# Kernel tuning notes

Hardware: AMD Instinct MI355X
Metric: run time of the kernel (lower is better)

## Reference

```python
import jax, jax.numpy as jnp
from jax import lax
import numpy as np

PARAM_SPECS = [
    ("w1", (16, 15, 5, 5)), ("b1", (16,)),
    ("w2", (32, 16, 3, 3)), ("b2", (32,)),
    ("w3", (32, 32, 3, 3)), ("b3", (32,)),
    ("w4", (32, 32, 3, 3)), ("b4", (32,)),
    ("w5", (64, 32, 3, 3)), ("b5", (64,)),
    ("w6", (32, 96, 3, 3)), ("b6", (32,)),
    ("w7", (32, 64, 3, 3)), ("b7", (32,)),
    ("w8", (32, 64, 3, 3)), ("b8", (32,)),
    ("w9", (64, 48, 3, 3)), ("b9", (64,)),
    ("wi", (16, 15, 3, 3)), ("bi", (16,)),
    ("wo", (3, 16, 3, 3)), ("bo", (3,)),
]


def conv2d(x, w, b, pad):
    y = lax.conv_general_dilated(x, w, (1, 1), [(pad, pad), (pad, pad)],
                                 dimension_numbers=("NCHW", "OIHW", "NCHW"))
    return y + b[None, :, None, None]


def maxpool2(x):
    return lax.reduce_window(x, -jnp.inf, lax.max, (1, 1, 2, 2), (1, 1, 2, 2), "VALID")


def upsample(x, hw):
    # bilinear, half-pixel centers == torch align_corners=False
    B, C = x.shape[:2]
    return jax.image.resize(x, (B, C, hw[0], hw[1]), method="bilinear")


def dcnn(img, p):
    x1 = jax.nn.relu(conv2d(img, p["w1"], p["b1"], 2))
    x2 = jax.nn.relu(conv2d(maxpool2(x1), p["w2"], p["b2"], 1))
    x3 = jax.nn.relu(conv2d(maxpool2(x2), p["w3"], p["b3"], 1))
    x4 = jax.nn.relu(conv2d(maxpool2(x3), p["w4"], p["b4"], 1))
    x5 = jax.nn.relu(conv2d(maxpool2(x4), p["w5"], p["b5"], 1))
    x6 = jax.nn.relu(conv2d(jnp.concatenate([upsample(x5, x4.shape[-2:]), x4], 1), p["w6"], p["b6"], 1))
    x7 = jax.nn.relu(conv2d(jnp.concatenate([upsample(x6, x3.shape[-2:]), x3], 1), p["w7"], p["b7"], 1))
    x8 = jax.nn.relu(conv2d(jnp.concatenate([upsample(x7, x2.shape[-2:]), x2], 1), p["w8"], p["b8"], 1))
    x9 = conv2d(jnp.concatenate([upsample(x8, x1.shape[-2:]), x1], 1), p["w9"], p["b9"], 1)
    return x9


def lrnn_op(X, P, axis, flip):
    # h_k = (1-P_k)*X_k + P_k*h_{k-1}, scanned along `axis`.
    # For reverse directions the torch code stacks hidden states in scan
    # order (spatially flipped) -> flip inputs, scan forward, keep order.
    if flip:
        X = jnp.flip(X, axis)
        P = jnp.flip(P, axis)
    xs = jnp.moveaxis(X, axis, 0)  # [L, B, 16, n]
    ps = jnp.moveaxis(P, axis, 0)

    def step(h, xp):
        x, p = xp
        h = (1.0 - p) * x + p * h
        return h, h

    h0 = jnp.zeros_like(xs[0])
    _, ys = lax.scan(step, h0, (xs, ps))
    return jnp.moveaxis(ys, 0, axis)


def lrnn_layer(x_in, fm):
    dirs = [(0, 3, False), (0, 3, True), (16, 2, False), (16, 2, True),
            (32, 3, False), (32, 3, True), (48, 2, False), (48, 2, True)]
    outs = [lrnn_op(x_in, fm[:, c:c + 16], axis, flip) for (c, axis, flip) in dirs]
    return jnp.max(jnp.stack(outs, axis=1), axis=1)


def setup_inputs() -> dict:
    key = jax.random.key(0)
    ks = jax.random.split(key, len(PARAM_SPECS) + 1)
    inp = {"img": jax.random.normal(ks[0], (8, 15, 256, 256), jnp.float32)}
    for i, (name, shape) in enumerate(PARAM_SPECS):
        inp[name] = jax.random.normal(ks[i + 1], shape, jnp.float32) * 0.05
    return inp


def reference(img, w1, b1, w2, b2, w3, b3, w4, b4, w5, b5, w6, b6, w7, b7,
              w8, b8, w9, b9, wi, bi, wo, bo):
    p = dict(w1=w1, b1=b1, w2=w2, b2=b2, w3=w3, b3=b3, w4=w4, b4=b4, w5=w5,
             b5=b5, w6=w6, b6=b6, w7=w7, b7=b7, w8=w8, b8=b8, w9=w9, b9=b9)
    fm = jnp.tanh(dcnn(img, p))          # [B,64,H,W]
    x_in = conv2d(img, wi, bi, 1)         # [B,16,H,W]
    out = lrnn_layer(x_in, fm)            # [B,16,H,W]
    return jax.nn.sigmoid(conv2d(out, wo, bo, 1))  # [B,3,H,W]
```

## Files before the change

kernel.cpp:

```cpp
#include <hip/hip_runtime.h>
#include <math.h>

typedef __attribute__((ext_vector_type(8)))  short bf16x8;
typedef __attribute__((ext_vector_type(8)))  unsigned short u16x8;
typedef __attribute__((ext_vector_type(16))) float f32x16;

__device__ __forceinline__ unsigned short f2bf(float f) {
    unsigned u = __float_as_uint(f);
    unsigned r = (u + 0x7FFFu + ((u >> 16) & 1u)) >> 16;
    return (unsigned short)r;
}
__device__ __forceinline__ float bf2f(unsigned short h) {
    return __uint_as_float(((unsigned)h) << 16);
}
__device__ __forceinline__ unsigned pack2(unsigned short a, unsigned short b) {
    return (unsigned)a | ((unsigned)b << 16);
}
__device__ __forceinline__ float fast_tanh(float x) {
    float e = __expf(2.f * x);
    return 1.f - 2.f / (e + 1.f);
}

__device__ __forceinline__ void bilin_setup(int y, int x, int Hi, int Wi,
                                            int& i00, int& i01, int& i10, int& i11,
                                            float& wy, float& wx)
{
    float fy = 0.5f * y - 0.25f;
    float fx = 0.5f * x - 0.25f;
    float y0f = floorf(fy), x0f = floorf(fx);
    wy = fy - y0f; wx = fx - x0f;
    int yA = (int)y0f, xA = (int)x0f;
    int yB = yA + 1, xB = xA + 1;
    yA = yA < 0 ? 0 : (yA > Hi - 1 ? Hi - 1 : yA);
    yB = yB < 0 ? 0 : (yB > Hi - 1 ? Hi - 1 : yB);
    xA = xA < 0 ? 0 : (xA > Wi - 1 ? Wi - 1 : xA);
    xB = xB < 0 ? 0 : (xB > Wi - 1 ? Wi - 1 : xB);
    i00 = yA * Wi + xA; i01 = yA * Wi + xB;
    i10 = yB * Wi + xA; i11 = yB * Wi + xB;
}

__device__ __forceinline__ void up2_setup(int v, int Hi, int& i0, int& i1, float& w)
{
    int a = (v - 1) >> 1;
    i0 = a < 0 ? 0 : a;
    int b = a + 1;
    i1 = b > Hi - 1 ? Hi - 1 : b;
    w = (v & 1) ? 0.25f : 0.75f;
}

__device__ __forceinline__ u16x8 bilin8(const unsigned short* __restrict__ sb,
                                        int i00, int i01, int i10, int i11,
                                        float wy, float wx, int stride)
{
    u16x8 v00 = *(const u16x8*)(sb + (size_t)i00 * stride);
    u16x8 v01 = *(const u16x8*)(sb + (size_t)i01 * stride);
    u16x8 v10 = *(const u16x8*)(sb + (size_t)i10 * stride);
    u16x8 v11 = *(const u16x8*)(sb + (size_t)i11 * stride);
    float w00 = (1.f - wy) * (1.f - wx), w01 = (1.f - wy) * wx;
    float w10 = wy * (1.f - wx),         w11 = wy * wx;
    u16x8 r;
#pragma unroll
    for (int j = 0; j < 8; ++j)
        r[j] = f2bf(w00 * bf2f(v00[j]) + w01 * bf2f(v01[j]) +
                    w10 * bf2f(v10[j]) + w11 * bf2f(v11[j]));
    return r;
}

__device__ const float ALPH[3][2][3][3] = {
    { { {0.f,0.f,0.f},      {0.f,1.f,0.f},       {0.f,0.75f,0.25f} },
      { {0.f,1.f,0.f},      {0.f,0.75f,0.25f},   {0.f,0.25f,0.75f} } },
    { { {0.75f,0.25f,0.f},  {0.25f,0.75f,0.f},   {0.f,0.75f,0.25f} },
      { {0.25f,0.75f,0.f},  {0.f,0.75f,0.25f},   {0.f,0.25f,0.75f} } },
    { { {0.75f,0.25f,0.f},  {0.25f,0.75f,0.f},   {0.f,1.f,0.f} },
      { {0.25f,0.75f,0.f},  {0.f,1.f,0.f},       {0.f,0.f,0.f} } }
};

__global__ void imgT_bf16(const float* __restrict__ img, unsigned short* __restrict__ dst)
{
    int idx = blockIdx.x * 256 + threadIdx.x;
    if (idx >= 8 * 256 * 256) return;
    int x = idx & 255, y = (idx >> 8) & 255, b = idx >> 16;
    unsigned short v[16];
#pragma unroll
    for (int c = 0; c < 15; ++c)
        v[c] = f2bf(img[(size_t)(b * 15 + c) * 65536 + y * 256 + x]);
    v[15] = 0;
    uint4 lo = make_uint4(pack2(v[0], v[1]), pack2(v[2], v[3]), pack2(v[4], v[5]), pack2(v[6], v[7]));
    uint4 hi = make_uint4(pack2(v[8], v[9]), pack2(v[10], v[11]), pack2(v[12], v[13]), pack2(v[14], v[15]));
    *(uint4*)(dst + (size_t)idx * 16)     = lo;
    *(uint4*)(dst + (size_t)idx * 16 + 8) = hi;
}

__device__ __forceinline__ void pack33(const float* __restrict__ w,
                                       unsigned short* __restrict__ dst,
                                       int i, int Cin, int Cout)
{
    int KST = Cin >> 4, MT = Cout >> 5;
    int j = i & 7;
    int lane = (i >> 3) & 63;
    int t = i >> 9;
    int mt = t % MT; t /= MT;
    int kst = t % KST;
    int s = t / KST;
    int oc = mt * 32 + (lane & 31);
    int ci = kst * 16 + (lane >> 5) * 8 + j;
    dst[i] = f2bf(w[(oc * Cin + ci) * 9 + s]);
}

__global__ void wprep_mega(const float* __restrict__ w9, const float* __restrict__ w8,
                           const float* __restrict__ w1, const float* __restrict__ wi,
                           const float* __restrict__ wo, const float* __restrict__ w2,
                           const float* __restrict__ w3, const float* __restrict__ w4,
                           const float* __restrict__ w5, const float* __restrict__ w6,
                           const float* __restrict__ w7,
                           unsigned short* __restrict__ wpk9, unsigned short* __restrict__ wpk8,
                           unsigned short* __restrict__ wpk1, unsigned short* __restrict__ wpki,
                           unsigned short* __restrict__ wpko, unsigned short* __restrict__ wpk2,
                           unsigned short* __restrict__ wpk3, unsigned short* __restrict__ wpk4,
                           unsigned short* __restrict__ wpk5, unsigned short* __restrict__ wpk6,
                           unsigned short* __restrict__ wpk7, unsigned short* __restrict__ wpk9e,
                           unsigned short* __restrict__ wpk8e)
{
    int idx = blockIdx.x * 256 + threadIdx.x;
    if (idx < 27648)       pack33(w9, wpk9, idx, 48, 64);
    else if (idx < 46080)  pack33(w8, wpk8, idx - 27648, 64, 32);
    else if (idx < 58880) {
        int i = idx - 46080;
        int j = i & 7;
        int lane = (i >> 3) & 63;
        int s = i >> 9;
        int oc = lane & 31;
        int ci = (lane >> 5) * 8 + j;
        float v = 0.f;
        if (oc < 16 && ci < 15) v = w1[((oc * 15 + ci) * 5 + s / 5) * 5 + s % 5];
        wpk1[i] = f2bf(v);
    } else if (idx < 63488) {
        int i = idx - 58880;
        int j = i & 7;
        int lane = (i >> 3) & 63;
        int s = i >> 9;
        int oc = lane & 31;
        int ci = (lane >> 5) * 8 + j;
        float v = 0.f;
        if (oc < 16 && ci < 15) v = wi[((oc * 15 + ci) * 3 + s / 3) * 3 + s % 3];
        wpki[i] = f2bf(v);
    } else if (idx < 68096) {
        int i = idx - 63488;
        int j = i & 7;
        int lane = (i >> 3) & 63;
        int s = i >> 9;
        int oc = lane & 31;
        int ci = (lane >> 5) * 8 + j;
        float v = 0.f;
        if (oc < 3) v = wo[((oc * 16 + ci) * 3 + s / 3) * 3 + s % 3];
        wpko[i] = f2bf(v);
    }
    else if (idx < 72704)  pack33(w2, wpk2, idx - 68096, 16, 32);
    else if (idx < 81920)  pack33(w3, wpk3, idx - 72704, 32, 32);
    else if (idx < 91136)  pack33(w4, wpk4, idx - 81920, 32, 32);
    else if (idx < 109568) pack33(w5, wpk5, idx - 91136, 32, 64);
    else if (idx < 137216) pack33(w6, wpk6, idx - 109568, 96, 32);
    else if (idx < 155648) pack33(w7, wpk7, idx - 137216, 64, 32);
    else if (idx < 266240) {
        int i = idx - 155648;
        int j = i & 7;
        int lane = (i >> 3) & 63;
        int t = i >> 9;
        int half = t & 1; t >>= 1;
        int kst  = t & 1; t >>= 1;
        int s    = t % 9; t /= 9;
        int py   = t & 1;
        int cls  = t >> 1;
        int dr = s / 3, dx = s % 3;
        int oc = half * 32 + (lane & 31);
        int ci = kst * 16 + (lane >> 5) * 8 + j;
        float v = 0.f;
#pragma unroll
        for (int dy = 0; dy < 3; ++dy)
            v += ALPH[cls][py][dy][dr] * w9[((oc * 48 + ci) * 3 + dy) * 3 + dx];
        wpk9e[i] = f2bf(v);
    }
    else if (idx < 321536) {
        int i = idx - 266240;
        int j = i & 7;
        int lane = (i >> 3) & 63;
        int t = i >> 9;
        int kst = t & 1; t >>= 1;
        int s   = t % 9; t /= 9;
        int py  = t & 1;
        int cls = t >> 1;
        int dr = s / 3, dx = s % 3;
        int oc = lane & 31;
        int ci = kst * 16 + (lane >> 5) * 8 + j;
        float v = 0.f;
#pragma unroll
        for (int dy = 0; dy < 3; ++dy)
            v += ALPH[cls][py][dy][dr] * w8[((oc * 64 + ci) * 3 + dy) * 3 + dx];
        wpk8e[i] = f2bf(v);
    }
}

template<int CIN, int COUT, int H, int W, int ROWS, int POOL>
__global__ __launch_bounds__(256)
void convN_mfma(const unsigned short* __restrict__ in,
                const unsigned short* __restrict__ wpk,
                const float* __restrict__ bias,
                unsigned short* __restrict__ out)
{
    constexpr int G = CIN / 8;
    constexpr int KST = CIN / 16;
    constexpr int MT = COUT / 32;
    constexpr int TR = ROWS + 2;
    constexpr int TWd = W + 2;
    constexpr int PS = TR * TWd * 8 + 8;
    __shared__ __align__(16) unsigned short smem[G * PS];

    const int tid  = threadIdx.x;
    const int lane = tid & 63;
    const int wv   = tid >> 6;
    const int q    = lane >> 5;
    const int y0   = blockIdx.x * ROWS;
    const int b    = blockIdx.y;

    for (int i = tid; i < G * TR * TWd; i += 256) {
        int g = i % G;
        int u = (i / G) % TWd;
        int t = i / (G * TWd);
        int yg = y0 + t - 1, xg = u - 1;
        u16x8 v = {0, 0, 0, 0, 0, 0, 0, 0};
        if (yg >= 0 && yg < H && xg >= 0 && xg < W) {
            if (POOL) {
                const unsigned short* q0 =
                    in + (((size_t)(b * 2 * H + 2 * yg) * 2 * W + 2 * xg) * CIN + g * 8);
                u16x8 a0 = *(const u16x8*)q0;
                u16x8 a1 = *(const u16x8*)(q0 + CIN);
                u16x8 a2 = *(const u16x8*)(q0 + (size_t)2 * W * CIN);
                u16x8 a3 = *(const u16x8*)(q0 + (size_t)2 * W * CIN + CIN);
#pragma unroll
                for (int j = 0; j < 8; ++j)
                    v[j] = f2bf(fmaxf(fmaxf(bf2f(a0[j]), bf2f(a1[j])),
                                      fmaxf(bf2f(a2[j]), bf2f(a3[j]))));
            } else {
                v = *(const u16x8*)(in + (((size_t)(b * H + yg) * W + xg) * CIN + g * 8));
            }
        }
        *(u16x8*)(&smem[g * PS + (t * TWd + u) * 8]) = v;
    }
    __syncthreads();

    const int p = wv * 32 + (lane & 31);
    const int r = p / W;
    const int x = p % W;

    f32x16 acc[MT];
#pragma unroll
    for (int mt = 0; mt < MT; ++mt)
#pragma unroll
        for (int i = 0; i < 16; ++i) acc[mt][i] = 0.f;

    const unsigned short* wbase = wpk + lane * 8;

#pragma unroll
    for (int s = 0; s < 9; ++s) {
        const int dy = s / 3, dx = s % 3;
#pragma unroll
        for (int kst = 0; kst < KST; ++kst) {
            const int g = kst * 2 + q;
            bf16x8 bfrag = *(const bf16x8*)(&smem[g * PS + ((r + dy) * TWd + (x + dx)) * 8]);
#pragma unroll
            for (int mt = 0; mt < MT; ++mt) {
                bf16x8 a = *(const bf16x8*)(wbase + ((s * KST + kst) * MT + mt) * 512);
                acc[mt] = __builtin_amdgcn_mfma_f32_32x32x16_bf16(a, bfrag, acc[mt], 0, 0, 0);
            }
        }
    }

    size_t base = ((size_t)(b * H + y0 + r) * W + x) * COUT;
#pragma unroll
    for (int mt = 0; mt < MT; ++mt)
#pragma unroll
        for (int rg = 0; rg < 4; ++rg) {
            int oc = mt * 32 + 8 * rg + 4 * q;
            unsigned short s0 = f2bf(fmaxf(acc[mt][rg * 4 + 0] + bias[oc + 0], 0.f));
            unsigned short s1 = f2bf(fmaxf(acc[mt][rg * 4 + 1] + bias[oc + 1], 0.f));
            unsigned short s2 = f2bf(fmaxf(acc[mt][rg * 4 + 2] + bias[oc + 2], 0.f));
            unsigned short s3 = f2bf(fmaxf(acc[mt][rg * 4 + 3] + bias[oc + 3], 0.f));
            *(uint2*)(out + base + oc) = make_uint2(pack2(s0, s1), pack2(s2, s3));
        }
}

template<int UPC, int CSKIP, int COUT, int H, int W, int ROWS>
__global__ __launch_bounds__(256)
void convU_mfma(const unsigned short* __restrict__ up,
                const unsigned short* __restrict__ skip,
                const unsigned short* __restrict__ wpk,
                const float* __restrict__ bias,
                unsigned short* __restrict__ out)
{
    constexpr int CIN = UPC + CSKIP;
    constexpr int G = CIN / 8;
    constexpr int GU = UPC / 8;
    constexpr int KST = CIN / 16;
    constexpr int MT = COUT / 32;
    constexpr int TR = ROWS + 2;
    constexpr int TWd = W + 2;
    constexpr int PS = TR * TWd * 8 + 8;
    __shared__ __align__(16) unsigned short smem[G * PS];

    const int tid  = threadIdx.x;
    const int lane = tid & 63;
    const int wv   = tid >> 6;
    const int q    = lane >> 5;
    const int y0   = blockIdx.x * ROWS;
    const int b    = blockIdx.y;

    for (int i = tid; i < G * TR * TWd; i += 256) {
        int g = i % G;
        int u = (i / G) % TWd;
        int t = i / (G * TWd);
        int yg = y0 + t - 1, xg = u - 1;
        u16x8 v = {0, 0, 0, 0, 0, 0, 0, 0};
        if (yg >= 0 && yg < H && xg >= 0 && xg < W) {
            if (g < GU) {
                int i00, i01, i10, i11; float wy, wx;
                bilin_setup(yg, xg, H / 2, W / 2, i00, i01, i10, i11, wy, wx);
                v = bilin8(up + (size_t)b * (H / 2) * (W / 2) * UPC + g * 8,
                           i00, i01, i10, i11, wy, wx, UPC);
            } else {
                v = *(const u16x8*)(skip + (((size_t)(b * H + yg) * W + xg) * CSKIP
                                            + (g - GU) * 8));
            }
        }
        *(u16x8*)(&smem[g * PS + (t * TWd + u) * 8]) = v;
    }
    __syncthreads();

    const int p = wv * 32 + (lane & 31);
    const int r = p / W;
    const int x = p % W;

    f32x16 acc[MT];
#pragma unroll
    for (int mt = 0; mt < MT; ++mt)
#pragma unroll
        for (int i = 0; i < 16; ++i) acc[mt][i] = 0.f;

    const unsigned short* wbase = wpk + lane * 8;

#pragma unroll
    for (int s = 0; s < 9; ++s) {
        const int dy = s / 3, dx = s % 3;
#pragma unroll
        for (int kst = 0; kst < KST; ++kst) {
            const int g = kst * 2 + q;
            bf16x8 bfrag = *(const bf16x8*)(&smem[g * PS + ((r + dy) * TWd + (x + dx)) * 8]);
#pragma unroll
            for (int mt = 0; mt < MT; ++mt) {
                bf16x8 a = *(const bf16x8*)(wbase + ((s * KST + kst) * MT + mt) * 512);
                acc[mt] = __builtin_amdgcn_mfma_f32_32x32x16_bf16(a, bfrag, acc[mt], 0, 0, 0);
            }
        }
    }

    size_t base = ((size_t)(b * H + y0 + r) * W + x) * COUT;
#pragma unroll
    for (int mt = 0; mt < MT; ++mt)
#pragma unroll
        for (int rg = 0; rg < 4; ++rg) {
            int oc = mt * 32 + 8 * rg + 4 * q;
            unsigned short s0 = f2bf(fmaxf(acc[mt][rg * 4 + 0] + bias[oc + 0], 0.f));
            unsigned short s1 = f2bf(fmaxf(acc[mt][rg * 4 + 1] + bias[oc + 1], 0.f));
            unsigned short s2 = f2bf(fmaxf(acc[mt][rg * 4 + 2] + bias[oc + 2], 0.f));
            unsigned short s3 = f2bf(fmaxf(acc[mt][rg * 4 + 3] + bias[oc + 3], 0.f));
            *(uint2*)(out + base + oc) = make_uint2(pack2(s0, s1), pack2(s2, s3));
        }
}

__global__ __launch_bounds__(256)
void conv1i_mfma(const unsigned short* __restrict__ imgT,
                 const unsigned short* __restrict__ wpk1,
                 const unsigned short* __restrict__ wpki,
                 const float* __restrict__ b1, const float* __restrict__ bi,
                 unsigned short* __restrict__ x1t, unsigned short* __restrict__ xin)
{
    __shared__ __align__(16) unsigned short smem[2 * 5 * 132 * 8];

    const int tid  = threadIdx.x;
    const int lane = tid & 63;
    const int wv   = tid >> 6;
    const int n    = lane & 31;
    const int q    = lane >> 5;
    const int y    = blockIdx.x >> 1;
    const int x0   = (blockIdx.x & 1) * 128;
    const int b    = blockIdx.y;

    for (int i = tid; i < 5 * 132 * 2; i += 256) {
        int r   = i / 264;
        int rem = i - r * 264;
        int xi  = rem >> 1;
        int g   = rem & 1;
        int yg = y + r - 2;
        int xg = x0 - 2 + xi;
        uint4 v = make_uint4(0, 0, 0, 0);
        if (yg >= 0 && yg < 256 && xg >= 0 && xg < 256)
            v = *(const uint4*)(imgT + (((size_t)(b * 256 + yg) * 256 + xg) * 16 + g * 8));
        *(uint4*)(&smem[((g * 5 + r) * 132 + xi) * 8]) = v;
    }
    __syncthreads();

    f32x16 acc1, acci;
#pragma unroll
    for (int i = 0; i < 16; ++i) { acc1[i] = 0.f; acci[i] = 0.f; }

    const int pxl = wv * 32 + n;
    const unsigned short* wb1 = wpk1 + lane * 8;
    const unsigned short* wbi = wpki + lane * 8;

#pragma unroll
    for (int s = 0; s < 25; ++s) {
        const int dy = s / 5, dx = s % 5;
        bf16x8 bfrag = *(const bf16x8*)(&smem[((q * 5 + dy) * 132 + pxl + dx) * 8]);
        bf16x8 a = *(const bf16x8*)(wb1 + s * 512);
        acc1 = __builtin_amdgcn_mfma_f32_32x32x16_bf16(a, bfrag, acc1, 0, 0, 0);
    }
#pragma unroll
    for (int s = 0; s < 9; ++s) {
        const int dy = s / 3, dx = s % 3;
        bf16x8 bfrag = *(const bf16x8*)(&smem[((q * 5 + dy + 1) * 132 + pxl + dx + 1) * 8]);
        bf16x8 a = *(const bf16x8*)(wbi + s * 512);
        acci = __builtin_amdgcn_mfma_f32_32x32x16_bf16(a, bfrag, acci, 0, 0, 0);
    }

    const int px = x0 + pxl;
    size_t base1 = ((size_t)(b * 256 + y) * 256 + px) * 16;
#pragma unroll
    for (int rg = 0; rg < 2; ++rg) {
        int oc = 8 * rg + 4 * q;
        unsigned short s0 = f2bf(fmaxf(acc1[rg * 4 + 0] + b1[oc + 0], 0.f));
        unsigned short s1 = f2bf(fmaxf(acc1[rg * 4 + 1] + b1[oc + 1], 0.f));
        unsigned short s2 = f2bf(fmaxf(acc1[rg * 4 + 2] + b1[oc + 2], 0.f));
        unsigned short s3 = f2bf(fmaxf(acc1[rg * 4 + 3] + b1[oc + 3], 0.f));
        *(uint2*)(x1t + base1 + oc) = make_uint2(pack2(s0, s1), pack2(s2, s3));
    }
#pragma unroll
    for (int reg = 0; reg < 8; ++reg) {
        int row = (reg & 3) + 8 * (reg >> 2) + 4 * q;
        xin[((size_t)(b * 16 + row) * 256 + y) * 256 + px] = f2bf(acci[reg] + bi[row]);
    }
}

__global__ __launch_bounds__(256)
void conv8_mfma(const unsigned short* __restrict__ x7t,
                const unsigned short* __restrict__ x2t,
                const unsigned short* __restrict__ wpk8,
                const unsigned short* __restrict__ wpk8e,
                const float* __restrict__ bias,
                unsigned short* __restrict__ x8t)
{
    constexpr int PSU = 3 * 66 * 8 + 8;
    constexpr int PSS = 4 * 66 * 8 + 8;
    constexpr int SOFF = 4 * PSU;
    __shared__ __align__(16) unsigned short smem[4 * PSU + 4 * PSS];

    const int tid  = threadIdx.x;
    const int lane = tid & 63;
    const int wv   = tid >> 6;
    const int n    = lane & 31;
    const int q    = lane >> 5;
    const int x0   = (blockIdx.x & 1) * 64;
    const int yp   = blockIdx.x >> 1;
    const int b    = blockIdx.y;

    for (int i = tid; i < 792 + 1056; i += 256) {
        if (i < 792) {
            int g   = i & 3;
            int rem = i >> 2;
            int xi  = rem % 66;
            int t8  = rem / 66;
            int r   = yp - 1 + t8;
            int xg  = x0 - 1 + xi;
            u16x8 v = {0, 0, 0, 0, 0, 0, 0, 0};
            if (r >= 0 && r < 64 && xg >= 0 && xg < 128) {
                int ix0, ix1; float wx;
                up2_setup(xg, 64, ix0, ix1, wx);
                const unsigned short* S = x7t + ((size_t)(b * 64 + r) * 64) * 32 + g * 8;
                u16x8 a0 = *(const u16x8*)(S + ix0 * 32);
                u16x8 a1 = *(const u16x8*)(S + ix1 * 32);
                float w1x = 1.f - wx;
#pragma unroll
                for (int j = 0; j < 8; ++j)
                    v[j] = f2bf(w1x * bf2f(a0[j]) + wx * bf2f(a1[j]));
            }
            *(u16x8*)(&smem[g * PSU + (t8 * 66 + xi) * 8]) = v;
        } else {
            int jI  = i - 792;
            int g   = jI & 3;
            int rem = jI >> 2;
            int xi  = rem % 66;
            int t   = rem / 66;
            int yg  = 2 * yp + t - 1;
            int xg  = x0 - 1 + xi;
            uint4 v = make_uint4(0, 0, 0, 0);
            if (yg >= 0 && yg < 128 && xg >= 0 && xg < 128)
                v = *(const uint4*)(x2t + (((size_t)(b * 128 + yg) * 128 + xg) * 32 + g * 8));
            *(uint4*)(&smem[SOFF + g * PSS + (t * 66 + xi) * 8]) = v;
        }
    }
    __syncthreads();

    const int rr  = wv >> 1;
    const int pxl = (wv & 1) * 32 + n;

    f32x16 acc;
#pragma unroll
    for (int i = 0; i < 16; ++i) acc[i] = 0.f;

    const int cls = (yp == 0) ? 0 : ((yp == 63) ? 2 : 1);
    const unsigned short* wE = wpk8e + (size_t)(cls * 2 + rr) * 9216 + lane * 8;
    const unsigned short* wS = wpk8 + lane * 8;

#pragma unroll
    for (int s = 0; s < 9; ++s) {
        const int dr = s / 3, dxx = s % 3;
#pragma unroll
        for (int kst = 0; kst < 2; ++kst) {
            const int g = kst * 2 + q;
            bf16x8 bfrag = *(const bf16x8*)(&smem[g * PSU + (dr * 66 + pxl + dxx) * 8]);
            bf16x8 a = *(const bf16x8*)(wE + (s * 2 + kst) * 512);
            acc = __builtin_amdgcn_mfma_f32_32x32x16_bf16(a, bfrag, acc, 0, 0, 0);
        }
#pragma unroll
        for (int kst = 0; kst < 2; ++kst) {
            const int g = kst * 2 + q;
            bf16x8 bfrag = *(const bf16x8*)(&smem[SOFF + g * PSS + ((rr + dr) * 66 + pxl + dxx) * 8]);
            bf16x8 a = *(const bf16x8*)(wS + (s * 4 + kst + 2) * 512);
            acc = __builtin_amdgcn_mfma_f32_32x32x16_bf16(a, bfrag, acc, 0, 0, 0);
        }
    }

    size_t base = ((size_t)(b * 128 + 2 * yp + rr) * 128 + x0 + pxl) * 32;
#pragma unroll
    for (int rg = 0; rg < 4; ++rg) {
        int oc0 = 8 * rg + 4 * q;
        unsigned short s0 = f2bf(fmaxf(acc[rg * 4 + 0] + bias[oc0 + 0], 0.f));
        unsigned short s1 = f2bf(fmaxf(acc[rg * 4 + 1] + bias[oc0 + 1], 0.f));
        unsigned short s2 = f2bf(fmaxf(acc[rg * 4 + 2] + bias[oc0 + 2], 0.f));
        unsigned short s3 = f2bf(fmaxf(acc[rg * 4 + 3] + bias[oc0 + 3], 0.f));
        *(uint2*)(x8t + base + oc0) = make_uint2(pack2(s0, s1), pack2(s2, s3));
    }
}

__global__ __launch_bounds__(256)
void conv9f_mfma(const unsigned short* __restrict__ x8t,
                 const unsigned short* __restrict__ x1t,
                 const unsigned short* __restrict__ wpk,
                 const unsigned short* __restrict__ wpk9e,
                 const float* __restrict__ bias,
                 unsigned short* __restrict__ fm)
{
    constexpr int PS8X = 3 * 66 * 8 + 8;
    constexpr int PS1  = 4 * 66 * 8 + 8;
    constexpr int X1OFF = 4 * PS8X;
    __shared__ __align__(16) unsigned short smem[4 * PS8X + 2 * PS1];

    const int tid  = threadIdx.x;
    const int lane = tid & 63;
    const int wv   = tid >> 6;
    const int n    = lane & 31;
    const int q    = lane >> 5;
    const int x0   = (blockIdx.x & 3) * 64;
    const int yp   = blockIdx.x >> 2;
    const int b    = blockIdx.y;

    for (int i = tid; i < 792 + 528; i += 256) {
        if (i < 792) {
            int g   = i & 3;
            int rem = i >> 2;
            int xi  = rem % 66;
            int t8  = rem / 66;
            int r   = yp - 1 + t8;
            int xg  = x0 - 1 + xi;
            u16x8 v = {0, 0, 0, 0, 0, 0, 0, 0};
            if (r >= 0 && r < 128 && xg >= 0 && xg < 256) {
                int ix0, ix1; float wx;
                up2_setup(xg, 128, ix0, ix1, wx);
                const unsigned short* S = x8t + ((size_t)(b * 128 + r) * 128) * 32 + g * 8;
                u16x8 a0 = *(const u16x8*)(S + ix0 * 32);
                u16x8 a1 = *(const u16x8*)(S + ix1 * 32);
                float w1x = 1.f - wx;
#pragma unroll
                for (int j = 0; j < 8; ++j)
                    v[j] = f2bf(w1x * bf2f(a0[j]) + wx * bf2f(a1[j]));
            }
            *(u16x8*)(&smem[g * PS8X + (t8 * 66 + xi) * 8]) = v;
        } else {
            int jI  = i - 792;
            int g   = jI & 1;
            int rem = jI >> 1;
            int xi  = rem % 66;
            int t   = rem / 66;
            int yg  = 2 * yp + t - 1;
            int xg  = x0 - 1 + xi;
            uint4 v = make_uint4(0, 0, 0, 0);
            if (yg >= 0 && yg < 256 && xg >= 0 && xg < 256)
                v = *(const uint4*)(x1t + (((size_t)(b * 256 + yg) * 256 + xg) * 16 + g * 8));
            *(uint4*)(&smem[X1OFF + g * PS1 + (t * 66 + xi) * 8]) = v;
        }
    }
    __syncthreads();

    const int rr  = wv >> 1;
    const int pxl = (wv & 1) * 32 + n;

    f32x16 acc0, acc1;
#pragma unroll
    for (int i = 0; i < 16; ++i) { acc0[i] = 0.f; acc1[i] = 0.f; }

    const int cls = (yp == 0) ? 0 : ((yp == 127) ? 2 : 1);
    const unsigned short* wE  = wpk9e + (size_t)(cls * 2 + rr) * 18432 + lane * 8;
    const unsigned short* w2b = wpk + lane * 8;

#pragma unroll
    for (int s = 0; s < 9; ++s) {
        const int dr = s / 3, dxx = s % 3;
#pragma unroll
        for (int kst = 0; kst < 2; ++kst) {
            const int g = kst * 2 + q;
            bf16x8 bfrag = *(const bf16x8*)(&smem[g * PS8X + (dr * 66 + pxl + dxx) * 8]);
            bf16x8 a0 = *(const bf16x8*)(wE + ((s * 2 + kst) * 2 + 0) * 512);
            bf16x8 a1 = *(const bf16x8*)(wE + ((s * 2 + kst) * 2 + 1) * 512);
            acc0 = __builtin_amdgcn_mfma_f32_32x32x16_bf16(a0, bfrag, acc0, 0, 0, 0);
            acc1 = __builtin_amdgcn_mfma_f32_32x32x16_bf16(a1, bfrag, acc1, 0, 0, 0);
        }
        {
            bf16x8 bfrag = *(const bf16x8*)(&smem[X1OFF + q * PS1 + ((rr + dr) * 66 + pxl + dxx) * 8]);
            bf16x8 a0 = *(const bf16x8*)(w2b + ((s * 3 + 2) * 2 + 0) * 512);
            bf16x8 a1 = *(const bf16x8*)(w2b + ((s * 3 + 2) * 2 + 1) * 512);
            acc0 = __builtin_amdgcn_mfma_f32_32x32x16_bf16(a0, bfrag, acc0, 0, 0, 0);
            acc1 = __builtin_amdgcn_mfma_f32_32x32x16_bf16(a1, bfrag, acc1, 0, 0, 0);
        }
    }

    __syncthreads();
    unsigned short* lout = smem;
    const int pb = rr * 64 + pxl + q * 512;
#pragma unroll
    for (int reg = 0; reg < 16; ++reg) {
        const int rbase = (reg & 3) + 8 * (reg >> 2);
        lout[rbase * 128 + pb]        = f2bf(fast_tanh(acc0[reg] + bias[rbase + 4 * q]));
        lout[(rbase + 32) * 128 + pb] = f2bf(fast_tanh(acc1[reg] + bias[rbase + 4 * q + 32]));
    }
    __syncthreads();

    const size_t fmb = (size_t)b * 64 * 65536 + (size_t)(2 * yp) * 256 + x0;
    for (int i = tid; i < 1024; i += 256) {
        int oc  = i >> 4;
        int p0  = (i & 15) * 8;
        int rr2 = p0 >> 6;
        int pl  = p0 & 63;
        uint4 v = *(const uint4*)(lout + oc * 128 + p0);
        *(uint4*)(fm + fmb + (size_t)oc * 65536 + rr2 * 256 + pl) = v;
    }
}

__device__ __forceinline__ int X2C(int x) { return x + (x >> 5); }

__global__ __launch_bounds__(256)
void lrnn_w_seg(const unsigned short* __restrict__ X, const unsigned short* __restrict__ FM,
                unsigned short* __restrict__ rnnW)
{
    __shared__ float tx[3][16][264];
    __shared__ unsigned short outm[2][16][256];
    __shared__ float segres[2][16][8][4];
    __shared__ float hin[2][16][8][2];

    const int tid = threadIdx.x;
    const int bid = blockIdx.x;
    const int yt = bid & 15;
    const int c  = (bid >> 4) & 15;
    const int b  = bid >> 8;
    const int y0 = yt * 16;

    const size_t xb  = ((size_t)(b * 16 + c) * 256 + y0) * 256;
    const size_t p1b = ((size_t)(b * 64 + c) * 256 + y0) * 256;
    const size_t p2b = ((size_t)(b * 64 + 32 + c) * 256 + y0) * 256;

    for (int i = tid; i < 1536; i += 256) {
        int s = i >> 9;
        int r = i & 511;
        int y = r >> 5;
        int g = r & 31;
        const unsigned short* sp = (s == 0) ? (X + xb) : (s == 1 ? FM + p1b : FM + p2b);
        u16x8 v = *(const u16x8*)(sp + (size_t)y * 256 + g * 8);
        int c0 = X2C(g * 8);
#pragma unroll
        for (int j = 0; j < 8; ++j) tx[s][y][c0 + j] = bf2f(v[j]);
    }
    __syncthreads();

    const int y  = tid & 15;
    const int sg = (tid >> 4) & 7;
    const int d  = tid >> 7;

    {
        float h1 = 0.f, h2 = 0.f, A1 = 1.f, A2 = 1.f;
        if (d == 0) {
            int cs = X2C(sg * 32);
#pragma unroll
            for (int i = 0; i < 32; ++i) {
                float xv = tx[0][y][cs + i], p1 = tx[1][y][cs + i], p2 = tx[2][y][cs + i];
                h1 = fmaf(p1, h1 - xv, xv); A1 *= p1;
                h2 = fmaf(p2, h2 - xv, xv); A2 *= p2;
            }
        } else {
            int cs = X2C(255 - sg * 32);
#pragma unroll
            for (int i = 0; i < 32; ++i) {
                float xv = tx[0][y][cs - i], p1 = tx[1][y][cs - i], p2 = tx[2][y][cs - i];
                h1 = fmaf(p1, h1 - xv, xv); A1 *= p1;
                h2 = fmaf(p2, h2 - xv, xv); A2 *= p2;
            }
        }
        segres[d][y][sg][0] = h1; segres[d][y][sg][1] = A1;
        segres[d][y][sg][2] = h2; segres[d][y][sg][3] = A2;
    }
    __syncthreads();

    if (tid < 32) {
        int yy = tid & 15, dd = tid >> 4;
        float c1 = 0.f, c2 = 0.f;
        for (int s = 0; s < 8; ++s) {
            hin[dd][yy][s][0] = c1;
            hin[dd][yy][s][1] = c2;
            c1 = segres[dd][yy][s][0] + segres[dd][yy][s][1] * c1;
            c2 = segres[dd][yy][s][2] + segres[dd][yy][s][3] * c2;
        }
    }
    __syncthreads();

    {
        float h1 = hin[d][y][sg][0], h2 = hin[d][y][sg][1];
        if (d == 0) {
            int cs = X2C(sg * 32);
            int xs = sg * 32;
#pragma unroll
            for (int i = 0; i < 32; ++i) {
                float xv = tx[0][y][cs + i], p1 = tx[1][y][cs + i], p2 = tx[2][y][cs + i];
                h1 = fmaf(p1, h1 - xv, xv);
                h2 = fmaf(p2, h2 - xv, xv);
                outm[0][y][xs + i] = f2bf(fmaxf(h1, h2));
            }
        } else {
            int cs = X2C(255 - sg * 32);
#pragma unroll
            for (int i = 0; i < 32; ++i) {
                int t = sg * 32 + i;
                float xv = tx[0][y][cs - i], p1 = tx[1][y][cs - i], p2 = tx[2][y][cs - i];
                h1 = fmaf(p1, h1 - xv, xv);
                h2 = fmaf(p2, h2 - xv, xv);
                outm[1][y][t] = f2bf(fmaxf(h1, h2));
            }
        }
    }
    __syncthreads();

    for (int i = tid; i < 4096; i += 256) {
        int x = i & 255, yy = i >> 8;
        float m = fmaxf(bf2f(outm[0][yy][x]), bf2f(outm[1][yy][x]));
        rnnW[xb + (size_t)yy * 256 + x] = f2bf(m);
    }
}

__global__ __launch_bounds__(256)
void lrnn_h_seg(const unsigned short* __restrict__ X, const unsigned short* __restrict__ FM,
                unsigned short* __restrict__ rnnH)
{
    __shared__ float tx[3][264][17];
    __shared__ unsigned short outm[2][256][16];
    __shared__ float segres[2][16][8][4];
    __shared__ float hin[2][16][8][2];

    const int tid = threadIdx.x;
    const int bid = blockIdx.x;
    const int xt = bid & 15;
    const int c  = (bid >> 4) & 15;
    const int b  = bid >> 8;
    const int x0 = xt * 16;

    const size_t xb  = (size_t)(b * 16 + c) * 65536 + x0;
    const size_t p1b = (size_t)(b * 64 + 16 + c) * 65536 + x0;
    const size_t p2b = (size_t)(b * 64 + 48 + c) * 65536 + x0;

    for (int i = tid; i < 1536; i += 256) {
        int s = i >> 9;
        int r = i & 511;
        int y = r >> 1;
        int g = r & 1;
        const unsigned short* sp = (s == 0) ? (X + xb) : (s == 1 ? FM + p1b : FM + p2b);
        u16x8 v = *(const u16x8*)(sp + (size_t)y * 256 + g * 8);
        int pr = y + (y >> 5);
#pragma unroll
        for (int j = 0; j < 8; ++j) tx[s][pr][g * 8 + j] = bf2f(v[j]);
    }
    __syncthreads();

    const int x  = tid & 15;
    const int sg = (tid >> 4) & 7;
    const int d  = tid >> 7;

    {
        float h1 = 0.f, h2 = 0.f, A1 = 1.f, A2 = 1.f;
        if (d == 0) {
            int rs = X2C(sg * 32);
#pragma unroll
            for (int i = 0; i < 32; ++i) {
                float xv = tx[0][rs + i][x], p1 = tx[1][rs + i][x], p2 = tx[2][rs + i][x];
                h1 = fmaf(p1, h1 - xv, xv); A1 *= p1;
                h2 = fmaf(p2, h2 - xv, xv); A2 *= p2;
            }
        } else {
            int rs = X2C(255 - sg * 32);
#pragma unroll
            for (int i = 0; i < 32; ++i) {
                float xv = tx[0][rs - i][x], p1 = tx[1][rs - i][x], p2 = tx[2][rs - i][x];
                h1 = fmaf(p1, h1 - xv, xv); A1 *= p1;
                h2 = fmaf(p2, h2 - xv, xv); A2 *= p2;
            }
        }
        segres[d][x][sg][0] = h1; segres[d][x][sg][1] = A1;
        segres[d][x][sg][2] = h2; segres[d][x][sg][3] = A2;
    }
    __syncthreads();

    if (tid < 32) {
        int xx = tid & 15, dd = tid >> 4;
        float c1 = 0.f, c2 = 0.f;
        for (int s = 0; s < 8; ++s) {
            hin[dd][xx][s][0] = c1;
            hin[dd][xx][s][1] = c2;
            c1 = segres[dd][xx][s][0] + segres[dd][xx][s][1] * c1;
            c2 = segres[dd][xx][s][2] + segres[dd][xx][s][3] * c2;
        }
    }
    __syncthreads();

    {
        float h1 = hin[d][x][sg][0], h2 = hin[d][x][sg][1];
        if (d == 0) {
            int rs = X2C(sg * 32);
            int ys = sg * 32;
#pragma unroll
            for (int i = 0; i < 32; ++i) {
                float xv = tx[0][rs + i][x], p1 = tx[1][rs + i][x], p2 = tx[2][rs + i][x];
                h1 = fmaf(p1, h1 - xv, xv);
                h2 = fmaf(p2, h2 - xv, xv);
                outm[0][ys + i][x] = f2bf(fmaxf(h1, h2));
            }
        } else {
            int rs = X2C(255 - sg * 32);
#pragma unroll
            for (int i = 0; i < 32; ++i) {
                int t = sg * 32 + i;
                float xv = tx[0][rs - i][x], p1 = tx[1][rs - i][x], p2 = tx[2][rs - i][x];
                h1 = fmaf(p1, h1 - xv, xv);
                h2 = fmaf(p2, h2 - xv, xv);
                outm[1][t][x] = f2bf(fmaxf(h1, h2));
            }
        }
    }
    __syncthreads();

    for (int i = tid; i < 4096; i += 256) {
        int xx = i & 15, yy = i >> 4;
        float m = fmaxf(bf2f(outm[0][yy][xx]), bf2f(outm[1][yy][xx]));
        rnnH[xb + (size_t)yy * 256 + xx] = f2bf(m);
    }
}

__global__ __launch_bounds__(256)
void convo_mfma(const unsigned short* __restrict__ rnnW,
                const unsigned short* __restrict__ rnnH,
                const unsigned short* __restrict__ wpko,
                const float* __restrict__ bo,
                float* __restrict__ outp)
{
    __shared__ __align__(16) unsigned short smem[2 * 3 * 130 * 8];

    const int tid  = threadIdx.x;
    const int lane = tid & 63;
    const int wv   = tid >> 6;
    const int n    = lane & 31;
    const int q    = lane >> 5;
    const int y    = blockIdx.x >> 1;
    const int x0   = (blockIdx.x & 1) * 128;
    const int b    = blockIdx.y;

    for (int i = tid; i < 3 * 16 * 17; i += 256) {
        int ch  = i & 15;
        int t   = i >> 4;
        int c   = t % 17;
        int r   = t / 17;
        int xi0 = c * 8;
        int yg  = y + r - 1;
        int g = ch >> 3, j = ch & 7;
        unsigned short* sb = &smem[((g * 3 + r) * 130) * 8 + j];
        if (yg >= 0 && yg < 256) {
            size_t off = (size_t)(b * 16 + ch) * 65536 + (size_t)yg * 256;
            int xg0 = x0 - 1 + xi0;
            if (xg0 >= 0 && xg0 + 7 < 256 && xi0 + 7 < 130) {
                u16x8 a  = *(const u16x8*)(rnnW + off + xg0);
                u16x8 bv = *(const u16x8*)(rnnH + off + xg0);
#pragma unroll
                for (int k = 0; k < 8; ++k)
                    sb[(xi0 + k) * 8] = bf2f(a[k]) >= bf2f(bv[k]) ? a[k] : bv[k];
            } else {
#pragma unroll
                for (int k = 0; k < 8; ++k) {
                    int xi = xi0 + k;
                    if (xi >= 130) break;
                    int xg = x0 - 1 + xi;
                    unsigned short m = 0;
                    if (xg >= 0 && xg < 256) {
                        unsigned short a = rnnW[off + xg], bvv = rnnH[off + xg];
                        m = bf2f(a) >= bf2f(bvv) ? a : bvv;
                    }
                    sb[xi * 8] = m;
                }
            }
        } else {
#pragma unroll
            for (int k = 0; k < 8; ++k) {
                int xi = xi0 + k;
                if (xi >= 130) break;
                sb[xi * 8] = 0;
            }
        }
    }
    __syncthreads();

    f32x16 acc;
#pragma unroll
    for (int i = 0; i < 16; ++i) acc[i] = 0.f;

    const int pxl = wv * 32 + n;
    const unsigned short* wbase = wpko + lane * 8;

#pragma unroll
    for (int s = 0; s < 9; ++s) {
        const int dy = s / 3, dx = s % 3;
        bf16x8 bfrag = *(const bf16x8*)(&smem[((q * 3 + dy) * 130 + pxl + dx) * 8]);
        bf16x8 a = *(const bf16x8*)(wbase + s * 512);
        acc = __builtin_amdgcn_mfma_f32_32x32x16_bf16(a, bfrag, acc, 0, 0, 0);
    }

    const int px = x0 + pxl;
    if (q == 0) {
#pragma unroll
        for (int oc = 0; oc < 3; ++oc) {
            float r = acc[oc] + bo[oc];
            outp[((size_t)(b * 3 + oc) * 256 + y) * 256 + px] = 1.f / (1.f + __expf(-r));
        }
    }
}

extern "C" void kernel_launch(void* const* d_in, const int* in_sizes, int n_in,
                              void* d_out, int out_size, void* d_ws, size_t ws_size,
                              hipStream_t stream)
{
    const float* img = (const float*)d_in[0];
    const float* w1 = (const float*)d_in[1];  const float* b1 = (const float*)d_in[2];
    const float* w2 = (const float*)d_in[3];  const float* b2 = (const float*)d_in[4];
    const float* w3 = (const float*)d_in[5];  const float* b3 = (const float*)d_in[6];
    const float* w4 = (const float*)d_in[7];  const float* b4 = (const float*)d_in[8];
    const float* w5 = (const float*)d_in[9];  const float* b5 = (const float*)d_in[10];
    const float* w6 = (const float*)d_in[11]; const float* b6 = (const float*)d_in[12];
    const float* w7 = (const float*)d_in[13]; const float* b7 = (const float*)d_in[14];
    const float* w8 = (const float*)d_in[15]; const float* b8 = (const float*)d_in[16];
    const float* w9 = (const float*)d_in[17]; const float* b9 = (const float*)d_in[18];
    const float* wi = (const float*)d_in[19]; const float* bi = (const float*)d_in[20];
    const float* wo = (const float*)d_in[21]; const float* bo = (const float*)d_in[22];

    char* wsb = (char*)d_ws;
    const size_t MB = (size_t)(1u << 20);
    unsigned short* imgT  = (unsigned short*)(wsb);
    unsigned short* x1t   = (unsigned short*)(wsb + 16 * MB);
    unsigned short* x2t   = (unsigned short*)(wsb + 32 * MB);
    unsigned short* x3t   = (unsigned short*)(wsb + 40 * MB);
    unsigned short* x4t   = (unsigned short*)(wsb + 42 * MB);
    unsigned short* x5t   = (unsigned short*)(wsb + 43 * MB);
    unsigned short* x6t   = (unsigned short*)(wsb + 46 * MB);
    unsigned short* x7t   = (unsigned short*)(wsb + 51 * MB);
    unsigned short* x8t   = (unsigned short*)(wsb + 70 * MB);
    unsigned short* fm16  = (unsigned short*)(wsb + 112 * MB);
    unsigned short* xin16 = (unsigned short*)(wsb + 176 * MB);
    unsigned short* rnnW  = (unsigned short*)(wsb);
    unsigned short* rnnH  = (unsigned short*)(wsb + 16 * MB);
    unsigned short* wpk9 = (unsigned short*)(wsb + 192 * MB);
    unsigned short* wpk8 = wpk9 + 27648;
    unsigned short* wpk1 = wpk8 + 18432;
    unsigned short* wpki = wpk1 + 12800;
    unsigned short* wpko = wpki + 4608;
    unsigned short* wpk2 = wpko + 4608;
    unsigned short* wpk3 = wpk2 + 4608;
    unsigned short* wpk4 = wpk3 + 9216;
    unsigned short* wpk5 = wpk4 + 9216;
    unsigned short* wpk6 = wpk5 + 18432;
    unsigned short* wpk7 = wpk6 + 27648;
    unsigned short* wpk9e = wpk7 + 18432;
    unsigned short* wpk8e = wpk9e + 110592;
    float* outp = (float*)d_out;

    wprep_mega<<<1256, 256, 0, stream>>>(w9, w8, w1, wi, wo, w2, w3, w4, w5, w6, w7,
                                         wpk9, wpk8, wpk1, wpki, wpko,
                                         wpk2, wpk3, wpk4, wpk5, wpk6, wpk7,
                                         wpk9e, wpk8e);
    imgT_bf16<<<2048, 256, 0, stream>>>(img, imgT);

    { dim3 grd(512, 8);
      conv1i_mfma<<<grd, 256, 0, stream>>>(imgT, wpk1, wpki, b1, bi, x1t, xin16); }

    convN_mfma<16, 32, 128, 128, 1, 1><<<dim3(128, 8), 256, 0, stream>>>(x1t, wpk2, b2, x2t);
    convN_mfma<32, 32, 64, 64, 2, 1><<<dim3(32, 8), 256, 0, stream>>>(x2t, wpk3, b3, x3t);
    convN_mfma<32, 32, 32, 32, 4, 1><<<dim3(8, 8), 256, 0, stream>>>(x3t, wpk4, b4, x4t);
    convN_mfma<32, 64, 16, 16, 8, 1><<<dim3(2, 8), 256, 0, stream>>>(x4t, wpk5, b5, x5t);

    convU_mfma<64, 32, 32, 32, 32, 4><<<dim3(8, 8), 256, 0, stream>>>(x5t, x4t, wpk6, b6, x6t);
    convU_mfma<32, 32, 32, 64, 64, 2><<<dim3(32, 8), 256, 0, stream>>>(x6t, x3t, wpk7, b7, x7t);
    { dim3 grd(128, 8);
      conv8_mfma<<<grd, 256, 0, stream>>>(x7t, x2t, wpk8, wpk8e, b8, x8t); }

    { dim3 grd(512, 8);
      conv9f_mfma<<<grd, 256, 0, stream>>>(x8t, x1t, wpk9, wpk9e, b9, fm16); }

    lrnn_w_seg<<<2048, 256, 0, stream>>>(xin16, fm16, rnnW);
    lrnn_h_seg<<<2048, 256, 0, stream>>>(xin16, fm16, rnnH);

    { dim3 grd(512, 8);
      convo_mfma<<<grd, 256, 0, stream>>>(rnnW, rnnH, wpko, bo, outp); }
}
```

Before: 413.8 us.

## Fuse W/H max into lrnn_h_seg and tile convo over four rows per block

lrnn_h_seg now reads the rnnW result and writes the elementwise max of both directions into one buffer, so the output conv reads a single tensor instead of two. convo_mfma now processes four output rows per block, with each wave handling one row across four 32-pixel tiles. This shares the 6-row halo in LDS and cuts the halo reload overhead from 3x to 1.5x. The trade-offs are an extra global read in lrnn_h_seg, scalar rather than vectorized loads in the convo staging loop, and 4x fewer blocks.

```diff
diff --git a/kernel.cpp b/kernel.cpp
--- a/kernel.cpp
+++ b/kernel.cpp
@@ -773,7 +773,7 @@
 
 __global__ __launch_bounds__(256)
 void lrnn_h_seg(const unsigned short* __restrict__ X, const unsigned short* __restrict__ FM,
-                unsigned short* __restrict__ rnnH)
+                const unsigned short* __restrict__ rnnW, unsigned short* __restrict__ rnnM)
 {
     __shared__ float tx[3][264][17];
     __shared__ unsigned short outm[2][256][16];
@@ -873,92 +873,68 @@
     for (int i = tid; i < 4096; i += 256) {
         int xx = i & 15, yy = i >> 4;
         float m = fmaxf(bf2f(outm[0][yy][xx]), bf2f(outm[1][yy][xx]));
-        rnnH[xb + (size_t)yy * 256 + xx] = f2bf(m);
+        size_t off = xb + (size_t)yy * 256 + xx;
+        m = fmaxf(m, bf2f(rnnW[off]));
+        rnnM[off] = f2bf(m);
     }
 }
 
 __global__ __launch_bounds__(256)
-void convo_mfma(const unsigned short* __restrict__ rnnW,
-                const unsigned short* __restrict__ rnnH,
+void convo_mfma(const unsigned short* __restrict__ rnnM,
                 const unsigned short* __restrict__ wpko,
                 const float* __restrict__ bo,
                 float* __restrict__ outp)
 {
-    __shared__ __align__(16) unsigned short smem[2 * 3 * 130 * 8];
+    constexpr int PSo = 6 * 130 * 8 + 8;
+    __shared__ __align__(16) unsigned short smem[2 * PSo];
 
     const int tid  = threadIdx.x;
     const int lane = tid & 63;
     const int wv   = tid >> 6;
     const int n    = lane & 31;
     const int q    = lane >> 5;
-    const int y    = blockIdx.x >> 1;
     const int x0   = (blockIdx.x & 1) * 128;
+    const int yq   = blockIdx.x >> 1;
     const int b    = blockIdx.y;
 
-    for (int i = tid; i < 3 * 16 * 17; i += 256) {
-        int ch  = i & 15;
-        int t   = i >> 4;
-        int c   = t % 17;
-        int r   = t / 17;
-        int xi0 = c * 8;
-        int yg  = y + r - 1;
+    for (int i = tid; i < 6 * 16 * 130; i += 256) {
+        int xi = i % 130;
+        int t  = i / 130;
+        int ch = t & 15;
+        int r  = t >> 4;
+        int yg = 4 * yq + r - 1;
+        int xg = x0 - 1 + xi;
+        unsigned short m = 0;
+        if (yg >= 0 && yg < 256 && xg >= 0 && xg < 256)
+            m = rnnM[(size_t)(b * 16 + ch) * 65536 + (size_t)yg * 256 + xg];
         int g = ch >> 3, j = ch & 7;
-        unsigned short* sb = &smem[((g * 3 + r) * 130) * 8 + j];
-        if (yg >= 0 && yg < 256) {
-            size_t off = (size_t)(b * 16 + ch) * 65536 + (size_t)yg * 256;
-            int xg0 = x0 - 1 + xi0;
-            if (xg0 >= 0 && xg0 + 7 < 256 && xi0 + 7 < 130) {
-                u16x8 a  = *(const u16x8*)(rnnW + off + xg0);
-                u16x8 bv = *(const u16x8*)(rnnH + off + xg0);
-#pragma unroll
-                for (int k = 0; k < 8; ++k)
-                    sb[(xi0 + k) * 8] = bf2f(a[k]) >= bf2f(bv[k]) ? a[k] : bv[k];
-            } else {
-#pragma unroll
-                for (int k = 0; k < 8; ++k) {
-                    int xi = xi0 + k;
-                    if (xi >= 130) break;
-                    int xg = x0 - 1 + xi;
-                    unsigned short m = 0;
-                    if (xg >= 0 && xg < 256) {
-                        unsigned short a = rnnW[off + xg], bvv = rnnH[off + xg];
-                        m = bf2f(a) >= bf2f(bvv) ? a : bvv;
-                    }
-                    sb[xi * 8] = m;
-                }
-            }
-        } else {
-#pragma unroll
-            for (int k = 0; k < 8; ++k) {
-                int xi = xi0 + k;
-                if (xi >= 130) break;
-                sb[xi * 8] = 0;
-            }
-        }
-    }
-    __syncthreads();
-
-    f32x16 acc;
-#pragma unroll
-    for (int i = 0; i < 16; ++i) acc[i] = 0.f;
-
-    const int pxl = wv * 32 + n;
+        smem[g * PSo + (r * 130 + xi) * 8 + j] = m;
+    }
+    __syncthreads();
+
     const unsigned short* wbase = wpko + lane * 8;
-
-#pragma unroll
-    for (int s = 0; s < 9; ++s) {
-        const int dy = s / 3, dx = s % 3;
-        bf16x8 bfrag = *(const bf16x8*)(&smem[((q * 3 + dy) * 130 + pxl + dx) * 8]);
-        bf16x8 a = *(const bf16x8*)(wbase + s * 512);
-        acc = __builtin_amdgcn_mfma_f32_32x32x16_bf16(a, bfrag, acc, 0, 0, 0);
-    }
-
-    const int px = x0 + pxl;
-    if (q == 0) {
-#pragma unroll
-        for (int oc = 0; oc < 3; ++oc) {
-            float r = acc[oc] + bo[oc];
-            outp[((size_t)(b * 3 + oc) * 256 + y) * 256 + px] = 1.f / (1.f + __expf(-r));
+    const int y = 4 * yq + wv;
+
+#pragma unroll
+    for (int xt = 0; xt < 4; ++xt) {
+        const int pxl = xt * 32 + n;
+        f32x16 acc;
+#pragma unroll
+        for (int i = 0; i < 16; ++i) acc[i] = 0.f;
+#pragma unroll
+        for (int s = 0; s < 9; ++s) {
+            const int dy = s / 3, dx = s % 3;
+            bf16x8 bfrag = *(const bf16x8*)(&smem[q * PSo + ((wv + dy) * 130 + pxl + dx) * 8]);
+            bf16x8 a = *(const bf16x8*)(wbase + s * 512);
+            acc = __builtin_amdgcn_mfma_f32_32x32x16_bf16(a, bfrag, acc, 0, 0, 0);
+        }
+        if (q == 0) {
+            const int px = x0 + pxl;
+#pragma unroll
+            for (int oc = 0; oc < 3; ++oc) {
+                float r2 = acc[oc] + bo[oc];
+                outp[((size_t)(b * 3 + oc) * 256 + y) * 256 + px] = 1.f / (1.f + __expf(-r2));
+            }
         }
     }
 }
@@ -994,7 +970,7 @@
     unsigned short* fm16  = (unsigned short*)(wsb + 112 * MB);
     unsigned short* xin16 = (unsigned short*)(wsb + 176 * MB);
     unsigned short* rnnW  = (unsigned short*)(wsb);
-    unsigned short* rnnH  = (unsigned short*)(wsb + 16 * MB);
+    unsigned short* rnnM  = (unsigned short*)(wsb + 16 * MB);
     unsigned short* wpk9 = (unsigned short*)(wsb + 192 * MB);
     unsigned short* wpk8 = wpk9 + 27648;
     unsigned short* wpk1 = wpk8 + 18432;
@@ -1033,8 +1009,8 @@
       conv9f_mfma<<<grd, 256, 0, stream>>>(x8t, x1t, wpk9, wpk9e, b9, fm16); }
 
     lrnn_w_seg<<<2048, 256, 0, stream>>>(xin16, fm16, rnnW);
-    lrnn_h_seg<<<2048, 256, 0, stream>>>(xin16, fm16, rnnH);
-
-    { dim3 grd(512, 8);
-      convo_mfma<<<grd, 256, 0, stream>>>(rnnW, rnnH, wpko, bo, outp); }
-}
+    lrnn_h_seg<<<2048, 256, 0, stream>>>(xin16, fm16, rnnW, rnnM);
+
+    { dim3 grd(128, 8);
+      convo_mfma<<<grd, 256, 0, stream>>>(rnnM, wpko, bo, outp); }
+}
```

After: 388.8 us. 6.0% less time.
